# Kernel optimization log

Hardware: AMD Instinct MI355X
Metric: run time of the kernel (lower is better)

Reference implementation:

```python
import jax, jax.numpy as jnp
import numpy as np
from jax import lax


def _gaussian_kernel(sigma=2.0, size=5):
    # matches torch: arange(-size//2 + 1, size//2 + 1) == [-2,-1,0,1,2] for size=5
    r = np.arange(-(size // 2), size // 2 + 1, dtype=np.float32)
    xx, yy = np.meshgrid(r, r, indexing='ij')
    k = np.exp(-(xx ** 2 + yy ** 2) / (2.0 * sigma ** 2))
    return jnp.asarray(k / k.sum(), dtype=jnp.float32)


SCHARR_0 = jnp.array([[3, 0, -3], [10, 0, -10], [3, 0, -3]], dtype=jnp.float32)
SCHARR_90 = jnp.array([[3, 10, 3], [0, 0, 0], [-3, -10, -3]], dtype=jnp.float32)
LAPLACIAN = jnp.array([[0, -1, 0], [-1, 4, -1], [0, -1, 0]], dtype=jnp.float32)
GAUSS = _gaussian_kernel(2.0, 5)
SCHARR_W = 1.0
LAP_W = 0.1


def dwconv(x, k, pad):
    # depthwise conv: x [B,C,H,W], k [kh,kw] shared across channels
    C = x.shape[1]
    kern = jnp.broadcast_to(k[None, None], (C, 1) + k.shape)
    return lax.conv_general_dilated(
        x, kern, window_strides=(1, 1), padding=[(pad, pad), (pad, pad)],
        feature_group_count=C, dimension_numbers=('NCHW', 'OIHW', 'NCHW'))


def conv1x1(x, w, b):
    # x [B,C,H,W], w [O,C], b [O]
    return jnp.einsum('bchw,oc->bohw', x, w) + b[None, :, None, None]


def setup_inputs() -> dict:
    key = jax.random.key(0)
    ks = jax.random.split(key, 6)
    B, C, H, W = 4, 256, 256, 256
    s = 0.05
    return {
        'x': jax.random.normal(ks[0], (B, C, H, W), jnp.float32),
        'w_in': jax.random.normal(ks[1], (64, 256), jnp.float32) * s,
        'b_in': jnp.zeros((64,), jnp.float32),
        'w_fc1': jax.random.normal(ks[2], (4, 64), jnp.float32) * s,
        'b_fc1': jnp.zeros((4,), jnp.float32),
        'w_fc2': jax.random.normal(ks[3], (64, 4), jnp.float32) * s,
        'b_fc2': jnp.zeros((64,), jnp.float32),
        'w_out': jax.random.normal(ks[4], (64, 64), jnp.float32) * s,
        'b_out': jnp.zeros((64,), jnp.float32),
    }


def reference(x, w_in, b_in, w_fc1, b_fc1, w_fc2, b_fc2, w_out, b_out):
    x = conv1x1(x, w_in, b_in)                       # [B,64,H,W]
    sm = dwconv(x, GAUSS, pad=2)                     # gaussian blur
    g0 = dwconv(sm, SCHARR_0, pad=1)
    g90 = dwconv(sm, SCHARR_90, pad=1)
    scharr_mag = SCHARR_W * jnp.maximum(jnp.abs(g0), jnp.abs(g90))
    lap = LAP_W * jnp.abs(dwconv(sm, LAPLACIAN, pad=1))
    edge = scharr_mag + lap
    edge = jnp.clip(edge / (edge.max() + 1e-8), 0.0, 1.0)
    # channel attention (SE)
    pooled = edge.mean(axis=(2, 3), keepdims=True)   # [B,64,1,1]
    h = jax.nn.relu(conv1x1(pooled, w_fc1, b_fc1))
    scale = jax.nn.sigmoid(conv1x1(h, w_fc2, b_fc2))
    edge = edge * scale
    return conv1x1(edge, w_out, b_out)
```

## Files before the change

### kernel.cpp

```cpp
#include <hip/hip_runtime.h>
#include <math.h>


#define HW 65536

#define WS_WT    0ull
#define WS_Y     65536ull
#define WS_EDGE  (65536ull + 67108864ull)
#define WS_SMALL (65536ull + 134217728ull)

__global__ __launch_bounds__(256) void k0_prep(const float* __restrict__ w_in,
                                               float* __restrict__ wT) {
    const int tid = threadIdx.x;
    for (int i = tid; i < 64 * 256; i += 256) {
        int o = i >> 8, c = i & 255;
        wT[c * 64 + o] = w_in[i];
    }
}

#define CH_COMP(xv, wrow)                                                     \
    {                                                                         \
        float4 w0 = *(const float4*)(wrow);                                   \
        float4 w1 = *(const float4*)((wrow) + 4);                             \
        float4 w2 = *(const float4*)((wrow) + 8);                             \
        float4 w3 = *(const float4*)((wrow) + 12);                            \
        float wf[16] = {w0.x,w0.y,w0.z,w0.w, w1.x,w1.y,w1.z,w1.w,             \
                        w2.x,w2.y,w2.z,w2.w, w3.x,w3.y,w3.z,w3.w};            \
        _Pragma("unroll")                                                     \
        for (int oi = 0; oi < 16; ++oi) {                                     \
            acc[0][oi] = fmaf((xv).x, wf[oi], acc[0][oi]);                    \
            acc[1][oi] = fmaf((xv).y, wf[oi], acc[1][oi]);                    \
            acc[2][oi] = fmaf((xv).z, wf[oi], acc[2][oi]);                    \
            acc[3][oi] = fmaf((xv).w, wf[oi], acc[3][oi]);                    \
        }                                                                     \
    }

__global__ __launch_bounds__(256) void k1_convin(const float* __restrict__ x,
                                                 const float* __restrict__ wT,
                                                 const float* __restrict__ b_in,
                                                 float* __restrict__ y) {
    const int tid  = threadIdx.x;
    const int lane = tid & 63;
    const int og   = __builtin_amdgcn_readfirstlane((tid >> 6) << 4);
    const int blk  = blockIdx.x;
    const int b    = blk >> 8;
    const int px   = ((blk & 255) << 8) + (lane << 2);

    const float* xp  = x + (size_t)(b << 8) * HW + px;
    const float* wTg = wT + og;

    float acc[4][16];
#pragma unroll
    for (int oi = 0; oi < 16; ++oi) {
        float bv = b_in[og + oi];
        acc[0][oi] = bv; acc[1][oi] = bv; acc[2][oi] = bv; acc[3][oi] = bv;
    }

    float4 xr0 = *(const float4*)(xp + 0 * (size_t)HW);
    float4 xr1 = *(const float4*)(xp + 1 * (size_t)HW);
    float4 xr2 = *(const float4*)(xp + 2 * (size_t)HW);
    float4 xr3 = *(const float4*)(xp + 3 * (size_t)HW);
    float4 xr4 = *(const float4*)(xp + 4 * (size_t)HW);
    float4 xr5 = *(const float4*)(xp + 5 * (size_t)HW);
    float4 xr6 = *(const float4*)(xp + 6 * (size_t)HW);
    float4 xr7 = *(const float4*)(xp + 7 * (size_t)HW);

#pragma unroll 1
    for (int cc = 0; cc < 256; cc += 8) {
        {
            const int gn = (cc + 8) & 255;
            float4 n0 = *(const float4*)(xp + (size_t)(gn    ) * HW);
            float4 n1 = *(const float4*)(xp + (size_t)(gn + 1) * HW);
            float4 n2 = *(const float4*)(xp + (size_t)(gn + 2) * HW);
            float4 n3 = *(const float4*)(xp + (size_t)(gn + 3) * HW);
            CH_COMP(xr0, wTg + (size_t)(cc    ) * 64);
            CH_COMP(xr1, wTg + (size_t)(cc + 1) * 64);
            CH_COMP(xr2, wTg + (size_t)(cc + 2) * 64);
            CH_COMP(xr3, wTg + (size_t)(cc + 3) * 64);
            xr0 = n0; xr1 = n1; xr2 = n2; xr3 = n3;
        }
        {
            const int gn = (cc + 12) & 255;
            float4 n0 = *(const float4*)(xp + (size_t)(gn    ) * HW);
            float4 n1 = *(const float4*)(xp + (size_t)(gn + 1) * HW);
            float4 n2 = *(const float4*)(xp + (size_t)(gn + 2) * HW);
            float4 n3 = *(const float4*)(xp + (size_t)(gn + 3) * HW);
            CH_COMP(xr4, wTg + (size_t)(cc + 4) * 64);
            CH_COMP(xr5, wTg + (size_t)(cc + 5) * 64);
            CH_COMP(xr6, wTg + (size_t)(cc + 6) * 64);
            CH_COMP(xr7, wTg + (size_t)(cc + 7) * 64);
            xr4 = n0; xr5 = n1; xr6 = n2; xr7 = n3;
        }
    }

    float* yb = y + (size_t)(b << 6) * HW + px;
#pragma unroll
    for (int oi = 0; oi < 16; ++oi)
        *(float4*)(yb + (size_t)(og + oi) * HW) = float4{acc[0][oi], acc[1][oi],
                                                         acc[2][oi], acc[3][oi]};
}

__global__ __launch_bounds__(256) void k2_edge(const float* __restrict__ y,
                                               float* __restrict__ edge,
                                               float* __restrict__ wavemax,
                                               float* __restrict__ wavesum) {
    const int lane = threadIdx.x & 63;
    const int task = blockIdx.x * 4 + (threadIdx.x >> 6);
    const int plane = task >> 4;
    const int r0 = (task & 15) << 4;
    const float* yp = y + (size_t)plane * HW;
    float* ep = edge + (size_t)plane * HW;
    const int col4 = lane << 2;

    const float g = 0.60653066f, G = 0.88249690f;
    const float S1 = 2.f * g + 2.f * G + 1.f;
    const float inv2 = 1.f / (S1 * S1);

    float4 h0{}, h1{}, h2{}, h3{}, h4{};
    float4 s0{}, s1{}, s2{};
    float lmax = 0.f, lsum = 0.f;

    float4 vcur{};
    if (r0 - 3 >= 0) vcur = *(const float4*)(yp + (r0 - 3) * 256 + col4);

    for (int j = r0 - 3; j <= r0 + 18; ++j) {
        float4 vnext{};
        const int jn = j + 1;
        if (jn <= r0 + 18 && jn >= 0 && jn < 256)
            vnext = *(const float4*)(yp + jn * 256 + col4);
        float4 v = vcur;
        float lz = __shfl(v.z, lane - 1), lw = __shfl(v.w, lane - 1);
        float rx = __shfl(v.x, lane + 1), ry = __shfl(v.y, lane + 1);
        if (lane == 0)  { lz = 0.f; lw = 0.f; }
        if (lane == 63) { rx = 0.f; ry = 0.f; }
        float4 hv;
        hv.x = fmaf(g, lz,  fmaf(G, lw,  fmaf(G, v.y, fmaf(g, v.z, v.x))));
        hv.y = fmaf(g, lw,  fmaf(G, v.x, fmaf(G, v.z, fmaf(g, v.w, v.y))));
        hv.z = fmaf(g, v.x, fmaf(G, v.y, fmaf(G, v.w, fmaf(g, rx, v.z))));
        hv.w = fmaf(g, v.y, fmaf(G, v.z, fmaf(G, rx,  fmaf(g, ry, v.w))));
        h0 = h1; h1 = h2; h2 = h3; h3 = h4; h4 = hv;

        if (j >= r0 + 1) {
            float4 sv;
            sv.x = (g * (h0.x + h4.x) + G * (h1.x + h3.x) + h2.x) * inv2;
            sv.y = (g * (h0.y + h4.y) + G * (h1.y + h3.y) + h2.y) * inv2;
            sv.z = (g * (h0.z + h4.z) + G * (h1.z + h3.z) + h2.z) * inv2;
            sv.w = (g * (h0.w + h4.w) + G * (h1.w + h3.w) + h2.w) * inv2;
            s0 = s1; s1 = s2; s2 = sv;

            if (j >= r0 + 3) {
                const int er = j - 3;
                float4 A = s0, B = s1, C = s2;
                float Alw = __shfl(A.w, lane - 1), Arx = __shfl(A.x, lane + 1);
                float Blw = __shfl(B.w, lane - 1), Brx = __shfl(B.x, lane + 1);
                float Clw = __shfl(C.w, lane - 1), Crx = __shfl(C.x, lane + 1);
                if (lane == 0)  { Alw = 0.f; Blw = 0.f; Clw = 0.f; }
                if (lane == 63) { Arx = 0.f; Brx = 0.f; Crx = 0.f; }
                if (er == 0)   { A = float4{}; Alw = 0.f; Arx = 0.f; }
                if (er == 255) { C = float4{}; Clw = 0.f; Crx = 0.f; }
                float A6[6] = {Alw, A.x, A.y, A.z, A.w, Arx};
                float B6[6] = {Blw, B.x, B.y, B.z, B.w, Brx};
                float C6[6] = {Clw, C.x, C.y, C.z, C.w, Crx};
                float4 e4;
                float* ev = (float*)&e4;
#pragma unroll
                for (int k = 0; k < 4; ++k) {
                    float g0  = 3.f * (A6[k] - A6[k+2]) + 10.f * (B6[k] - B6[k+2])
                              + 3.f * (C6[k] - C6[k+2]);
                    float g90 = 3.f * (A6[k] - C6[k]) + 10.f * (A6[k+1] - C6[k+1])
                              + 3.f * (A6[k+2] - C6[k+2]);
                    float lap = 4.f * B6[k+1] - B6[k] - B6[k+2] - A6[k+1] - C6[k+1];
                    float e = fmaxf(fabsf(g0), fabsf(g90)) + 0.1f * fabsf(lap);
                    ev[k] = e;
                    lmax = fmaxf(lmax, e);
                    lsum += e;
                }
                *(float4*)(ep + er * 256 + col4) = e4;
            }
        }
        vcur = vnext;
    }

    for (int off = 32; off > 0; off >>= 1) {
        lmax = fmaxf(lmax, __shfl_down(lmax, off));
        lsum += __shfl_down(lsum, off);
    }
    if (lane == 0) {
        wavemax[task] = lmax;
        wavesum[task] = lsum;
    }
}

__global__ __launch_bounds__(256) void k3_se(const float* __restrict__ wavemax,
                                             const float* __restrict__ wavesum,
                                             const float* __restrict__ w_fc1,
                                             const float* __restrict__ b_fc1,
                                             const float* __restrict__ w_fc2,
                                             const float* __restrict__ b_fc2,
                                             const float* __restrict__ w_out,
                                             float* __restrict__ w_eff) {
    const int tid = threadIdx.x;
    const int b = tid >> 6, o = tid & 63;
    __shared__ float smax[256];
    __shared__ float ssum[256];
    __shared__ float coef[256];

    float m = 0.f;
    for (int i = tid; i < 4096; i += 256) m = fmaxf(m, wavemax[i]);
    smax[tid] = m;
    float ps = 0.f;
#pragma unroll
    for (int k = 0; k < 16; ++k) ps += wavesum[tid * 16 + k];
    ssum[tid] = ps;
    __syncthreads();
    for (int s = 128; s > 0; s >>= 1) {
        if (tid < s) smax[tid] = fmaxf(smax[tid], smax[tid + s]);
        __syncthreads();
    }
    const float mx = smax[0];
    const float inv = 1.f / (mx + 1e-8f);

    float h[4];
#pragma unroll
    for (int j = 0; j < 4; ++j) h[j] = b_fc1[j];
    for (int c = 0; c < 64; ++c) {
        float pooled = ssum[b * 64 + c] * inv * (1.f / 65536.f);
#pragma unroll
        for (int j = 0; j < 4; ++j) h[j] = fmaf(pooled, w_fc1[j * 64 + c], h[j]);
    }
#pragma unroll
    for (int j = 0; j < 4; ++j) h[j] = fmaxf(h[j], 0.f);
    float z = b_fc2[o];
#pragma unroll
    for (int j = 0; j < 4; ++j) z = fmaf(h[j], w_fc2[o * 4 + j], z);
    float sc = 1.f / (1.f + expf(-z));
    coef[tid] = sc * inv;
    __syncthreads();
    for (int c = 0; c < 64; ++c)
        w_eff[((b * 64) + c) * 64 + o] = w_out[o * 64 + c] * coef[b * 64 + c];
}

__global__ __launch_bounds__(256) void k4_out(const float* __restrict__ edge,
                                              const float* __restrict__ w_eff,
                                              const float* __restrict__ b_out,
                                              float* __restrict__ out) {
    const int tid  = threadIdx.x;
    const int lane = tid & 63;
    const int og   = __builtin_amdgcn_readfirstlane((tid >> 6) << 4);
    const int blk  = blockIdx.x;
    const int b    = blk >> 8;
    const int px   = ((blk & 255) << 8) + (lane << 2);

    const float* eb  = edge + (size_t)(b << 6) * HW + px;
    const float* wTg = w_eff + (b << 12) + og;

    float acc[4][16];
#pragma unroll
    for (int oi = 0; oi < 16; ++oi) {
        float bv = b_out[og + oi];
        acc[0][oi] = bv; acc[1][oi] = bv; acc[2][oi] = bv; acc[3][oi] = bv;
    }

    float4 xr0 = *(const float4*)(eb + 0 * (size_t)HW);
    float4 xr1 = *(const float4*)(eb + 1 * (size_t)HW);
    float4 xr2 = *(const float4*)(eb + 2 * (size_t)HW);
    float4 xr3 = *(const float4*)(eb + 3 * (size_t)HW);
    float4 xr4 = *(const float4*)(eb + 4 * (size_t)HW);
    float4 xr5 = *(const float4*)(eb + 5 * (size_t)HW);
    float4 xr6 = *(const float4*)(eb + 6 * (size_t)HW);
    float4 xr7 = *(const float4*)(eb + 7 * (size_t)HW);

#pragma unroll 1
    for (int cc = 0; cc < 64; cc += 8) {
        {
            const int gn = (cc + 8) & 63;
            float4 n0 = *(const float4*)(eb + (size_t)(gn    ) * HW);
            float4 n1 = *(const float4*)(eb + (size_t)(gn + 1) * HW);
            float4 n2 = *(const float4*)(eb + (size_t)(gn + 2) * HW);
            float4 n3 = *(const float4*)(eb + (size_t)(gn + 3) * HW);
            CH_COMP(xr0, wTg + (size_t)(cc    ) * 64);
            CH_COMP(xr1, wTg + (size_t)(cc + 1) * 64);
            CH_COMP(xr2, wTg + (size_t)(cc + 2) * 64);
            CH_COMP(xr3, wTg + (size_t)(cc + 3) * 64);
            xr0 = n0; xr1 = n1; xr2 = n2; xr3 = n3;
        }
        {
            const int gn = (cc + 12) & 63;
            float4 n0 = *(const float4*)(eb + (size_t)(gn    ) * HW);
            float4 n1 = *(const float4*)(eb + (size_t)(gn + 1) * HW);
            float4 n2 = *(const float4*)(eb + (size_t)(gn + 2) * HW);
            float4 n3 = *(const float4*)(eb + (size_t)(gn + 3) * HW);
            CH_COMP(xr4, wTg + (size_t)(cc + 4) * 64);
            CH_COMP(xr5, wTg + (size_t)(cc + 5) * 64);
            CH_COMP(xr6, wTg + (size_t)(cc + 6) * 64);
            CH_COMP(xr7, wTg + (size_t)(cc + 7) * 64);
            xr4 = n0; xr5 = n1; xr6 = n2; xr7 = n3;
        }
    }

    float* ob = out + (size_t)(b << 6) * HW + px;
#pragma unroll
    for (int oi = 0; oi < 16; ++oi)
        *(float4*)(ob + (size_t)(og + oi) * HW) = float4{acc[0][oi], acc[1][oi],
                                                         acc[2][oi], acc[3][oi]};
}

extern "C" void kernel_launch(void* const* d_in, const int* in_sizes, int n_in,
                              void* d_out, int out_size, void* d_ws, size_t ws_size,
                              hipStream_t stream) {
    const float* x     = (const float*)d_in[0];
    const float* w_in  = (const float*)d_in[1];
    const float* b_in  = (const float*)d_in[2];
    const float* w_fc1 = (const float*)d_in[3];
    const float* b_fc1 = (const float*)d_in[4];
    const float* w_fc2 = (const float*)d_in[5];
    const float* b_fc2 = (const float*)d_in[6];
    const float* w_out = (const float*)d_in[7];
    const float* b_out = (const float*)d_in[8];

    char* ws = (char*)d_ws;
    float* wT      = (float*)(ws + WS_WT);
    float* y       = (float*)(ws + WS_Y);
    float* edge    = (float*)(ws + WS_EDGE);
    float* wavemax = (float*)(ws + WS_SMALL);
    float* wavesum = (float*)(ws + WS_SMALL + 16384);
    float* w_eff   = (float*)(ws + WS_SMALL + 32768);
    float* out     = (float*)d_out;

    hipLaunchKernelGGL(k0_prep,  dim3(1),    dim3(256), 0, stream, w_in, wT);
    hipLaunchKernelGGL(k1_convin,dim3(1024), dim3(256), 0, stream, x, wT, b_in, y);
    hipLaunchKernelGGL(k2_edge,  dim3(1024), dim3(256), 0, stream, y, edge, wavemax, wavesum);
    hipLaunchKernelGGL(k3_se,    dim3(1),    dim3(256), 0, stream, wavemax, wavesum,
                       w_fc1, b_fc1, w_fc2, b_fc2, w_out, w_eff);
    hipLaunchKernelGGL(k4_out,   dim3(1024), dim3(256), 0, stream, edge, w_eff, b_out, out);
}
```

Baseline: 494.0 us.

## Retile 1x1 convs so each thread computes all 64 outputs for two pixels

The input and output 1x1 convolution kernels now give each thread 2 pixels by 64 output channels instead of 4 pixels by 16 output channels. Each input value is then read from global memory only once per block rather than once per wave, removing the fourfold redundant x/edge reads. The costs are 128 accumulators per thread, narrower float2 loads, half as many blocks, and more weight loads per input element, so register pressure and occupancy may suffer.

```diff
diff --git a/kernel.cpp b/kernel.cpp
--- a/kernel.cpp
+++ b/kernel.cpp
@@ -18,20 +18,19 @@
     }
 }
 
-#define CH_COMP(xv, wrow)                                                     \
+#define CH64(xv, wrow)                                                        \
     {                                                                         \
-        float4 w0 = *(const float4*)(wrow);                                   \
-        float4 w1 = *(const float4*)((wrow) + 4);                             \
-        float4 w2 = *(const float4*)((wrow) + 8);                             \
-        float4 w3 = *(const float4*)((wrow) + 12);                            \
-        float wf[16] = {w0.x,w0.y,w0.z,w0.w, w1.x,w1.y,w1.z,w1.w,             \
-                        w2.x,w2.y,w2.z,w2.w, w3.x,w3.y,w3.z,w3.w};            \
         _Pragma("unroll")                                                     \
-        for (int oi = 0; oi < 16; ++oi) {                                     \
-            acc[0][oi] = fmaf((xv).x, wf[oi], acc[0][oi]);                    \
-            acc[1][oi] = fmaf((xv).y, wf[oi], acc[1][oi]);                    \
-            acc[2][oi] = fmaf((xv).z, wf[oi], acc[2][oi]);                    \
-            acc[3][oi] = fmaf((xv).w, wf[oi], acc[3][oi]);                    \
+        for (int o4 = 0; o4 < 16; ++o4) {                                     \
+            float4 w = *(const float4*)((wrow) + 4 * o4);                     \
+            acc0[4*o4+0] = fmaf((xv).x, w.x, acc0[4*o4+0]);                   \
+            acc0[4*o4+1] = fmaf((xv).x, w.y, acc0[4*o4+1]);                   \
+            acc0[4*o4+2] = fmaf((xv).x, w.z, acc0[4*o4+2]);                   \
+            acc0[4*o4+3] = fmaf((xv).x, w.w, acc0[4*o4+3]);                   \
+            acc1[4*o4+0] = fmaf((xv).y, w.x, acc1[4*o4+0]);                   \
+            acc1[4*o4+1] = fmaf((xv).y, w.y, acc1[4*o4+1]);                   \
+            acc1[4*o4+2] = fmaf((xv).y, w.z, acc1[4*o4+2]);                   \
+            acc1[4*o4+3] = fmaf((xv).y, w.w, acc1[4*o4+3]);                   \
         }                                                                     \
     }
 
@@ -39,65 +38,43 @@
                                                  const float* __restrict__ wT,
                                                  const float* __restrict__ b_in,
                                                  float* __restrict__ y) {
-    const int tid  = threadIdx.x;
-    const int lane = tid & 63;
-    const int og   = __builtin_amdgcn_readfirstlane((tid >> 6) << 4);
-    const int blk  = blockIdx.x;
-    const int b    = blk >> 8;
-    const int px   = ((blk & 255) << 8) + (lane << 2);
-
-    const float* xp  = x + (size_t)(b << 8) * HW + px;
-    const float* wTg = wT + og;
-
-    float acc[4][16];
-#pragma unroll
-    for (int oi = 0; oi < 16; ++oi) {
-        float bv = b_in[og + oi];
-        acc[0][oi] = bv; acc[1][oi] = bv; acc[2][oi] = bv; acc[3][oi] = bv;
-    }
-
-    float4 xr0 = *(const float4*)(xp + 0 * (size_t)HW);
-    float4 xr1 = *(const float4*)(xp + 1 * (size_t)HW);
-    float4 xr2 = *(const float4*)(xp + 2 * (size_t)HW);
-    float4 xr3 = *(const float4*)(xp + 3 * (size_t)HW);
-    float4 xr4 = *(const float4*)(xp + 4 * (size_t)HW);
-    float4 xr5 = *(const float4*)(xp + 5 * (size_t)HW);
-    float4 xr6 = *(const float4*)(xp + 6 * (size_t)HW);
-    float4 xr7 = *(const float4*)(xp + 7 * (size_t)HW);
+    const int tid = threadIdx.x;
+    const int blk = blockIdx.x;
+    const int b   = blk >> 7;
+    const int px  = ((blk & 127) << 9) + (tid << 1);
+
+    const float* xp = x + (size_t)(b << 8) * HW + px;
+
+    float acc0[64], acc1[64];
+#pragma unroll
+    for (int o = 0; o < 64; ++o) {
+        float bv = b_in[o];
+        acc0[o] = bv; acc1[o] = bv;
+    }
+
+    float2 xr0 = *(const float2*)(xp + 0 * (size_t)HW);
+    float2 xr1 = *(const float2*)(xp + 1 * (size_t)HW);
+    float2 xr2 = *(const float2*)(xp + 2 * (size_t)HW);
+    float2 xr3 = *(const float2*)(xp + 3 * (size_t)HW);
 
 #pragma unroll 1
-    for (int cc = 0; cc < 256; cc += 8) {
-        {
-            const int gn = (cc + 8) & 255;
-            float4 n0 = *(const float4*)(xp + (size_t)(gn    ) * HW);
-            float4 n1 = *(const float4*)(xp + (size_t)(gn + 1) * HW);
-            float4 n2 = *(const float4*)(xp + (size_t)(gn + 2) * HW);
-            float4 n3 = *(const float4*)(xp + (size_t)(gn + 3) * HW);
-            CH_COMP(xr0, wTg + (size_t)(cc    ) * 64);
-            CH_COMP(xr1, wTg + (size_t)(cc + 1) * 64);
-            CH_COMP(xr2, wTg + (size_t)(cc + 2) * 64);
-            CH_COMP(xr3, wTg + (size_t)(cc + 3) * 64);
-            xr0 = n0; xr1 = n1; xr2 = n2; xr3 = n3;
-        }
-        {
-            const int gn = (cc + 12) & 255;
-            float4 n0 = *(const float4*)(xp + (size_t)(gn    ) * HW);
-            float4 n1 = *(const float4*)(xp + (size_t)(gn + 1) * HW);
-            float4 n2 = *(const float4*)(xp + (size_t)(gn + 2) * HW);
-            float4 n3 = *(const float4*)(xp + (size_t)(gn + 3) * HW);
-            CH_COMP(xr4, wTg + (size_t)(cc + 4) * 64);
-            CH_COMP(xr5, wTg + (size_t)(cc + 5) * 64);
-            CH_COMP(xr6, wTg + (size_t)(cc + 6) * 64);
-            CH_COMP(xr7, wTg + (size_t)(cc + 7) * 64);
-            xr4 = n0; xr5 = n1; xr6 = n2; xr7 = n3;
-        }
+    for (int cc = 0; cc < 256; cc += 4) {
+        const int gn = (cc + 4) & 255;
+        float2 n0 = *(const float2*)(xp + (size_t)(gn    ) * HW);
+        float2 n1 = *(const float2*)(xp + (size_t)(gn + 1) * HW);
+        float2 n2 = *(const float2*)(xp + (size_t)(gn + 2) * HW);
+        float2 n3 = *(const float2*)(xp + (size_t)(gn + 3) * HW);
+        CH64(xr0, wT + (size_t)(cc    ) * 64);
+        CH64(xr1, wT + (size_t)(cc + 1) * 64);
+        CH64(xr2, wT + (size_t)(cc + 2) * 64);
+        CH64(xr3, wT + (size_t)(cc + 3) * 64);
+        xr0 = n0; xr1 = n1; xr2 = n2; xr3 = n3;
     }
 
     float* yb = y + (size_t)(b << 6) * HW + px;
 #pragma unroll
-    for (int oi = 0; oi < 16; ++oi)
-        *(float4*)(yb + (size_t)(og + oi) * HW) = float4{acc[0][oi], acc[1][oi],
-                                                         acc[2][oi], acc[3][oi]};
+    for (int o = 0; o < 64; ++o)
+        *(float2*)(yb + (size_t)o * HW) = float2{acc0[o], acc1[o]};
 }
 
 __global__ __launch_bounds__(256) void k2_edge(const float* __restrict__ y,
@@ -244,65 +221,44 @@
                                               const float* __restrict__ w_eff,
                                               const float* __restrict__ b_out,
                                               float* __restrict__ out) {
-    const int tid  = threadIdx.x;
-    const int lane = tid & 63;
-    const int og   = __builtin_amdgcn_readfirstlane((tid >> 6) << 4);
-    const int blk  = blockIdx.x;
-    const int b    = blk >> 8;
-    const int px   = ((blk & 255) << 8) + (lane << 2);
-
-    const float* eb  = edge + (size_t)(b << 6) * HW + px;
-    const float* wTg = w_eff + (b << 12) + og;
-
-    float acc[4][16];
-#pragma unroll
-    for (int oi = 0; oi < 16; ++oi) {
-        float bv = b_out[og + oi];
-        acc[0][oi] = bv; acc[1][oi] = bv; acc[2][oi] = bv; acc[3][oi] = bv;
-    }
-
-    float4 xr0 = *(const float4*)(eb + 0 * (size_t)HW);
-    float4 xr1 = *(const float4*)(eb + 1 * (size_t)HW);
-    float4 xr2 = *(const float4*)(eb + 2 * (size_t)HW);
-    float4 xr3 = *(const float4*)(eb + 3 * (size_t)HW);
-    float4 xr4 = *(const float4*)(eb + 4 * (size_t)HW);
-    float4 xr5 = *(const float4*)(eb + 5 * (size_t)HW);
-    float4 xr6 = *(const float4*)(eb + 6 * (size_t)HW);
-    float4 xr7 = *(const float4*)(eb + 7 * (size_t)HW);
+    const int tid = threadIdx.x;
+    const int blk = blockIdx.x;
+    const int b   = blk >> 7;
+    const int px  = ((blk & 127) << 9) + (tid << 1);
+
+    const float* eb = edge + (size_t)(b << 6) * HW + px;
+    const float* wb = w_eff + (b << 12);
+
+    float acc0[64], acc1[64];
+#pragma unroll
+    for (int o = 0; o < 64; ++o) {
+        float bv = b_out[o];
+        acc0[o] = bv; acc1[o] = bv;
+    }
+
+    float2 xr0 = *(const float2*)(eb + 0 * (size_t)HW);
+    float2 xr1 = *(const float2*)(eb + 1 * (size_t)HW);
+    float2 xr2 = *(const float2*)(eb + 2 * (size_t)HW);
+    float2 xr3 = *(const float2*)(eb + 3 * (size_t)HW);
 
 #pragma unroll 1
-    for (int cc = 0; cc < 64; cc += 8) {
-        {
-            const int gn = (cc + 8) & 63;
-            float4 n0 = *(const float4*)(eb + (size_t)(gn    ) * HW);
-            float4 n1 = *(const float4*)(eb + (size_t)(gn + 1) * HW);
-            float4 n2 = *(const float4*)(eb + (size_t)(gn + 2) * HW);
-            float4 n3 = *(const float4*)(eb + (size_t)(gn + 3) * HW);
-            CH_COMP(xr0, wTg + (size_t)(cc    ) * 64);
-            CH_COMP(xr1, wTg + (size_t)(cc + 1) * 64);
-            CH_COMP(xr2, wTg + (size_t)(cc + 2) * 64);
-            CH_COMP(xr3, wTg + (size_t)(cc + 3) * 64);
-            xr0 = n0; xr1 = n1; xr2 = n2; xr3 = n3;
-        }
-        {
-            const int gn = (cc + 12) & 63;
-            float4 n0 = *(const float4*)(eb + (size_t)(gn    ) * HW);
-            float4 n1 = *(const float4*)(eb + (size_t)(gn + 1) * HW);
-            float4 n2 = *(const float4*)(eb + (size_t)(gn + 2) * HW);
-            float4 n3 = *(const float4*)(eb + (size_t)(gn + 3) * HW);
-            CH_COMP(xr4, wTg + (size_t)(cc + 4) * 64);
-            CH_COMP(xr5, wTg + (size_t)(cc + 5) * 64);
-            CH_COMP(xr6, wTg + (size_t)(cc + 6) * 64);
-            CH_COMP(xr7, wTg + (size_t)(cc + 7) * 64);
-            xr4 = n0; xr5 = n1; xr6 = n2; xr7 = n3;
-        }
+    for (int cc = 0; cc < 64; cc += 4) {
+        const int gn = (cc + 4) & 63;
+        float2 n0 = *(const float2*)(eb + (size_t)(gn    ) * HW);
+        float2 n1 = *(const float2*)(eb + (size_t)(gn + 1) * HW);
+        float2 n2 = *(const float2*)(eb + (size_t)(gn + 2) * HW);
+        float2 n3 = *(const float2*)(eb + (size_t)(gn + 3) * HW);
+        CH64(xr0, wb + (size_t)(cc    ) * 64);
+        CH64(xr1, wb + (size_t)(cc + 1) * 64);
+        CH64(xr2, wb + (size_t)(cc + 2) * 64);
+        CH64(xr3, wb + (size_t)(cc + 3) * 64);
+        xr0 = n0; xr1 = n1; xr2 = n2; xr3 = n3;
     }
 
     float* ob = out + (size_t)(b << 6) * HW + px;
 #pragma unroll
-    for (int oi = 0; oi < 16; ++oi)
-        *(float4*)(ob + (size_t)(og + oi) * HW) = float4{acc[0][oi], acc[1][oi],
-                                                         acc[2][oi], acc[3][oi]};
+    for (int o = 0; o < 64; ++o)
+        *(float2*)(ob + (size_t)o * HW) = float2{acc0[o], acc1[o]};
 }
 
 extern "C" void kernel_launch(void* const* d_in, const int* in_sizes, int n_in,
@@ -327,10 +283,10 @@
     float* w_eff   = (float*)(ws + WS_SMALL + 32768);
     float* out     = (float*)d_out;
 
-    hipLaunchKernelGGL(k0_prep,  dim3(1),    dim3(256), 0, stream, w_in, wT);
-    hipLaunchKernelGGL(k1_convin,dim3(1024), dim3(256), 0, stream, x, wT, b_in, y);
-    hipLaunchKernelGGL(k2_edge,  dim3(1024), dim3(256), 0, stream, y, edge, wavemax, wavesum);
-    hipLaunchKernelGGL(k3_se,    dim3(1),    dim3(256), 0, stream, wavemax, wavesum,
+    hipLaunchKernelGGL(k0_prep,  dim3(1),   dim3(256), 0, stream, w_in, wT);
+    hipLaunchKernelGGL(k1_convin,dim3(512), dim3(256), 0, stream, x, wT, b_in, y);
+    hipLaunchKernelGGL(k2_edge,  dim3(1024),dim3(256), 0, stream, y, edge, wavemax, wavesum);
+    hipLaunchKernelGGL(k3_se,    dim3(1),   dim3(256), 0, stream, wavemax, wavesum,
                        w_fc1, b_fc1, w_fc2, b_fc2, w_out, w_eff);
-    hipLaunchKernelGGL(k4_out,   dim3(1024), dim3(256), 0, stream, edge, w_eff, b_out, out);
-}
+    hipLaunchKernelGGL(k4_out,   dim3(512), dim3(256), 0, stream, edge, w_eff, b_out, out);
+}
```

After: 573.1 us. +16.0%, slower.
